# Kernel tuning notes

Measured on AMD Instinct MI355X. Metric: run time of the kernel, lower is better.

The kernel has to match this reference:

```python
import jax, jax.numpy as jnp
import numpy as np

B, C, H, W = 32, 3, 512, 512
OUT = (64, 64)  # (out_grid[0]=Nx, out_grid[1]=Ny)
SMALL = 1e-4


def setup_inputs() -> dict:
    key = jax.random.key(0)
    k1, k2 = jax.random.split(key, 2)
    X = jax.random.normal(k1, (B, C, H, W), dtype=jnp.float32)
    fan_in = C * H * W
    # localization net: flatten + dense(5); scaled so p ~ N(0,1) and exp(p) is stable
    W_loc = jax.random.normal(k2, (fan_in, 5), dtype=jnp.float32) / np.float32(np.sqrt(fan_in))
    b_loc = jnp.zeros((5,), dtype=jnp.float32)
    return {"X": X, "W_loc": W_loc, "b_loc": b_loc}


def reference(X, W_loc, b_loc):
    Bn = X.shape[0]
    # locnet: p = flatten(X) @ W_loc + b_loc  -> [B, 5]
    p = X.reshape(Bn, -1) @ W_loc + b_loc

    N = min(OUT)
    gx = OUT[0] * (p[:, 0] + 1.0) / 2.0          # [B]
    gy = OUT[1] * (p[:, 1] + 1.0) / 2.0          # [B]
    sigma2 = jnp.exp(p[:, 2])                    # [B]
    delta = jnp.exp(p[:, 3]) * (max(W, H) - 1) / (N - 1.0)  # [B]
    gamma = jnp.exp(p[:, 4])                     # [B]

    i1 = jnp.arange(OUT[0], dtype=jnp.float32)   # [Nx]
    i2 = jnp.arange(OUT[1], dtype=jnp.float32)   # [Ny]
    a = jnp.arange(W, dtype=jnp.float32)         # [W]
    b = jnp.arange(H, dtype=jnp.float32)         # [H]

    mx = gx[:, None] + delta[:, None] * (i1 - N / 2.0 - 0.5)  # [B, Nx]
    my = gy[:, None] + delta[:, None] * (i2 - N / 2.0 - 0.5)  # [B, Ny]

    Fx = jnp.exp(-((a - mx[:, :, None]) ** 2) / (2.0 * sigma2[:, None, None]))  # [B,Nx,W]
    Fx = Fx / (Fx.sum(axis=-1, keepdims=True) + SMALL)
    Fy = jnp.exp(-((b - my[:, :, None]) ** 2) / (2.0 * sigma2[:, None, None]))  # [B,Ny,H]
    Fy = Fy / (Fy.sum(axis=-1, keepdims=True) + SMALL)

    # glimpse read: gamma * Fy @ X @ Fx^T, done as batched contractions
    Fyx = jnp.einsum('bnh,bchw->bcnw', Fy, X)        # [B,C,Ny,W]
    out = jnp.einsum('bcnw,bmw->bcnm', Fyx, Fx)      # [B,C,Ny,Nx]
    return gamma[:, None, None, None] * out
```

## Files before the change

kernel.cpp:

```cpp
#include <hip/hip_runtime.h>
#include <math.h>

#define B_ 32
#define C_ 3
#define H_ 512
#define W_ 512
#define NOUT 64
#define FAN (C_*H_*W_)

#define CHUNKS 192
#define CELEMS (FAN / CHUNKS)
#define BGROUPS 4

#define PPART_STRIDE 160
#define GAMMA_OFF (CHUNKS * PPART_STRIDE)
#define PFLOATS 32768
#define FXH_U 0
#define FXL_U 1048576
#define FYH_U 2097152
#define FYL_U 3145728

typedef __bf16 bf16x8 __attribute__((ext_vector_type(8)));
typedef float f32x4 __attribute__((ext_vector_type(4)));

__device__ __forceinline__ unsigned short f2bf(float f) {
    unsigned int u = __float_as_uint(f);
    u = (u + 0x7FFFu + ((u >> 16) & 1u)) >> 16;
    return (unsigned short)u;
}
__device__ __forceinline__ float bf2f(unsigned short h) {
    return __uint_as_float(((unsigned int)h) << 16);
}
__device__ __forceinline__ unsigned int cvt_pk_bf16(float lo, float hi) {
    unsigned int r;
    asm("v_cvt_pk_bf16_f32 %0, %1, %2" : "=v"(r) : "v"(lo), "v"(hi));
    return r;
}

union BF8U { uint4 u; bf16x8 v; };

__global__ __launch_bounds__(256) void k_locnet(const float* __restrict__ X,
                                                const float* __restrict__ Wl,
                                                float* __restrict__ ws) {
    const int chunk = blockIdx.x;
    const int b0 = blockIdx.y * 8;
    const int t = threadIdx.x;

    float acc[8][5] = {};
    const size_t base = (size_t)chunk * CELEMS;

    for (int k = t; k < CELEMS / 4; k += 256) {
        const size_t i0 = base + (size_t)k * 4;
        const float4* W4 = (const float4*)(Wl + i0 * 5);
        float4 w0 = W4[0], w1 = W4[1], w2 = W4[2], w3 = W4[3], w4 = W4[4];
        float wv[20] = {w0.x, w0.y, w0.z, w0.w,
                        w1.x, w1.y, w1.z, w1.w,
                        w2.x, w2.y, w2.z, w2.w,
                        w3.x, w3.y, w3.z, w3.w,
                        w4.x, w4.y, w4.z, w4.w};
        #pragma unroll
        for (int bb = 0; bb < 8; bb++) {
            float4 x = *(const float4*)(X + (size_t)(b0 + bb) * FAN + i0);
            float xv[4] = {x.x, x.y, x.z, x.w};
            #pragma unroll
            for (int e = 0; e < 4; e++)
                #pragma unroll
                for (int j = 0; j < 5; j++)
                    acc[bb][j] += xv[e] * wv[e * 5 + j];
        }
    }

    #pragma unroll
    for (int off = 32; off > 0; off >>= 1)
        #pragma unroll
        for (int bb = 0; bb < 8; bb++)
            #pragma unroll
            for (int j = 0; j < 5; j++)
                acc[bb][j] += __shfl_down(acc[bb][j], off);

    __shared__ float sred[4][40];
    const int wave = t >> 6, lane = t & 63;
    if (lane == 0) {
        #pragma unroll
        for (int bb = 0; bb < 8; bb++)
            #pragma unroll
            for (int j = 0; j < 5; j++)
                sred[wave][bb * 5 + j] = acc[bb][j];
    }
    __syncthreads();
    if (t < 40) {
        float s = sred[0][t] + sred[1][t] + sred[2][t] + sred[3][t];
        ws[(size_t)chunk * PPART_STRIDE + b0 * 5 + t] = s;
    }
}

__global__ __launch_bounds__(256) void k_filters(const float* __restrict__ bl,
                                                 float* __restrict__ ws,
                                                 float* __restrict__ out) {
    const int n = blockIdx.x;
    const int b = blockIdx.y;
    const int which = blockIdx.z;
    const int t = threadIdx.x;

    {
        const int bid = blockIdx.x + NOUT * (blockIdx.y + B_ * blockIdx.z);
        if (t < 24) {
            ((float4*)out)[(size_t)bid * 24 + t] = make_float4(0.f, 0.f, 0.f, 0.f);
        }
    }

    float pj[5] = {0.f, 0.f, 0.f, 0.f, 0.f};
    if (t < CHUNKS) {
        const float* pr = ws + (size_t)t * PPART_STRIDE + b * 5;
        #pragma unroll
        for (int j = 0; j < 5; j++) pj[j] = pr[j];
    }
    #pragma unroll
    for (int off = 32; off > 0; off >>= 1)
        #pragma unroll
        for (int j = 0; j < 5; j++) pj[j] += __shfl_down(pj[j], off);

    __shared__ float spart[4][5];
    __shared__ float pfin[5];
    const int wave = t >> 6, lane = t & 63;
    if (lane == 0) {
        #pragma unroll
        for (int j = 0; j < 5; j++) spart[wave][j] = pj[j];
    }
    __syncthreads();
    if (t < 5) pfin[t] = spart[0][t] + spart[1][t] + spart[2][t] + spart[3][t] + bl[t];
    __syncthreads();

    const float p0 = pfin[0], p1 = pfin[1], p2 = pfin[2], p3 = pfin[3];
    if (which == 0 && n == 0 && t == 0) ws[GAMMA_OFF + b] = expf(pfin[4]);

    const float g = (which == 0) ? 32.f * (p0 + 1.f) : 32.f * (p1 + 1.f);
    const float sigma2 = expf(p2);
    const float inv2s = 0.5f / sigma2;
    const float delta = expf(p3) * (511.0f / 63.0f);
    const float mean = g + delta * ((float)n - 32.5f);

    float d0 = (float)(2 * t) - mean;
    float f0 = expf(-d0 * d0 * inv2s);
    float d1 = (float)(2 * t + 1) - mean;
    float f1 = expf(-d1 * d1 * inv2s);

    float s = f0 + f1;
    #pragma unroll
    for (int off = 32; off > 0; off >>= 1) s += __shfl_down(s, off);
    __shared__ float sred[4];
    __shared__ float stot;
    if (lane == 0) sred[wave] = s;
    __syncthreads();
    if (t == 0) stot = sred[0] + sred[1] + sred[2] + sred[3] + 1e-4f;
    __syncthreads();
    const float scale = 1.0f / stot;

    unsigned short* wsu = (unsigned short*)(ws + PFLOATS);
    unsigned int* dstH = (unsigned int*)(wsu + (which ? FYH_U : FXH_U) + ((size_t)b * NOUT + n) * 512);
    unsigned int* dstL = (unsigned int*)(wsu + (which ? FYL_U : FXL_U) + ((size_t)b * NOUT + n) * 512);

    float v0 = f0 * scale;
    float v1 = f1 * scale;
    unsigned short h0 = f2bf(v0);
    unsigned short h1 = f2bf(v1);
    unsigned short l0 = f2bf(v0 - bf2f(h0));
    unsigned short l1 = f2bf(v1 - bf2f(h1));
    dstH[t] = (unsigned int)h0 | ((unsigned int)h1 << 16);
    dstL[t] = (unsigned int)l0 | ((unsigned int)l1 << 16);
}

#define KC 64
#define PITCH 72
#define TSZ (64 * PITCH)

__global__ __launch_bounds__(256) void k_glimpse(const float* __restrict__ X,
                                                 const float* __restrict__ ws,
                                                 float* __restrict__ out) {
    const int hc = blockIdx.x;
    const int bc = blockIdx.y;
    const int b = bc / 3;
    const int t = threadIdx.x;
    const int lane = t & 63;
    const int wv = t >> 6;
    const int l15 = lane & 15;
    const int quad = lane >> 4;
    const int hbase = hc * 64;

    __shared__ __align__(16) unsigned short lds[4 * TSZ];
    unsigned short* Xh = lds;
    unsigned short* Xl = lds + TSZ;
    unsigned short* Fh = lds + 2 * TSZ;
    unsigned short* Fl = lds + 3 * TSZ;

    const float* Xp = X + (size_t)bc * (H_ * W_) + (size_t)hbase * W_;
    const unsigned short* wsu = (const unsigned short*)(ws + PFLOATS);
    const unsigned short* FxHp = wsu + FXH_U + (size_t)b * NOUT * 512;
    const unsigned short* FxLp = wsu + FXL_U + (size_t)b * NOUT * 512;
    const unsigned short* FyHp = wsu + FYH_U + (size_t)b * NOUT * 512;
    const unsigned short* FyLp = wsu + FYL_U + (size_t)b * NOUT * 512;

    const float* xlane = Xp + (size_t)(16 * wv + l15) * W_ + quad * 8;

    const int srow0 = t >> 3;
    const int sc8 = (t & 7) * 8;

    {
        uint4 h0 = *(const uint4*)(FxHp + (size_t)srow0 * 512 + sc8);
        uint4 l0 = *(const uint4*)(FxLp + (size_t)srow0 * 512 + sc8);
        uint4 h1 = *(const uint4*)(FxHp + (size_t)(srow0 + 32) * 512 + sc8);
        uint4 l1 = *(const uint4*)(FxLp + (size_t)(srow0 + 32) * 512 + sc8);
        *(uint4*)&Fh[srow0 * PITCH + sc8] = h0;
        *(uint4*)&Fl[srow0 * PITCH + sc8] = l0;
        *(uint4*)&Fh[(srow0 + 32) * PITCH + sc8] = h1;
        *(uint4*)&Fl[(srow0 + 32) * PITCH + sc8] = l1;
    }
    __syncthreads();

    f32x4 acc[4] = {};

    #pragma unroll
    for (int wt = 0; wt < 8; wt++) {
        unsigned short* curH = (wt & 1) ? Xh : Fh;
        unsigned short* curL = (wt & 1) ? Xl : Fl;
        unsigned short* nxtH = (wt & 1) ? Fh : Xh;
        unsigned short* nxtL = (wt & 1) ? Fl : Xl;

        uint4 nh0, nl0, nh1, nl1;
        if (wt < 7) {
            const int wb = (wt + 1) * KC;
            nh0 = *(const uint4*)(FxHp + (size_t)srow0 * 512 + wb + sc8);
            nl0 = *(const uint4*)(FxLp + (size_t)srow0 * 512 + wb + sc8);
            nh1 = *(const uint4*)(FxHp + (size_t)(srow0 + 32) * 512 + wb + sc8);
            nl1 = *(const uint4*)(FxLp + (size_t)(srow0 + 32) * 512 + wb + sc8);
        }

        #pragma unroll
        for (int ks = 0; ks < 2; ks++) {
            const float* xp = xlane + wt * KC + ks * 32;
            float4 x0 = *(const float4*)(xp);
            float4 x1 = *(const float4*)(xp + 4);
            BF8U ah, al;
            ah.u.x = cvt_pk_bf16(x0.x, x0.y);
            ah.u.y = cvt_pk_bf16(x0.z, x0.w);
            ah.u.z = cvt_pk_bf16(x1.x, x1.y);
            ah.u.w = cvt_pk_bf16(x1.z, x1.w);
            al.u.x = cvt_pk_bf16(x0.x - __uint_as_float(ah.u.x << 16),
                                 x0.y - __uint_as_float(ah.u.x & 0xffff0000u));
            al.u.y = cvt_pk_bf16(x0.z - __uint_as_float(ah.u.y << 16),
                                 x0.w - __uint_as_float(ah.u.y & 0xffff0000u));
            al.u.z = cvt_pk_bf16(x1.x - __uint_as_float(ah.u.z << 16),
                                 x1.y - __uint_as_float(ah.u.z & 0xffff0000u));
            al.u.w = cvt_pk_bf16(x1.z - __uint_as_float(ah.u.w << 16),
                                 x1.w - __uint_as_float(ah.u.w & 0xffff0000u));

            const int ko = ks * 32 + quad * 8;
            #pragma unroll
            for (int mt = 0; mt < 4; mt++) {
                bf16x8 bh = *(const bf16x8*)&curH[(16 * mt + l15) * PITCH + ko];
                bf16x8 bl2 = *(const bf16x8*)&curL[(16 * mt + l15) * PITCH + ko];
                acc[mt] = __builtin_amdgcn_mfma_f32_16x16x32_bf16(ah.v, bh, acc[mt], 0, 0, 0);
                acc[mt] = __builtin_amdgcn_mfma_f32_16x16x32_bf16(al.v, bh, acc[mt], 0, 0, 0);
                acc[mt] = __builtin_amdgcn_mfma_f32_16x16x32_bf16(ah.v, bl2, acc[mt], 0, 0, 0);
            }
        }

        if (wt < 7) {
            *(uint4*)&nxtH[srow0 * PITCH + sc8] = nh0;
            *(uint4*)&nxtL[srow0 * PITCH + sc8] = nl0;
            *(uint4*)&nxtH[(srow0 + 32) * PITCH + sc8] = nh1;
            *(uint4*)&nxtL[(srow0 + 32) * PITCH + sc8] = nl1;
        }
        __syncthreads();
    }

    #pragma unroll
    for (int mt = 0; mt < 4; mt++) {
        float g0 = acc[mt][0], g1 = acc[mt][1], g2 = acc[mt][2], g3 = acc[mt][3];
        unsigned int h01 = cvt_pk_bf16(g0, g1);
        unsigned int h23 = cvt_pk_bf16(g2, g3);
        float r0 = __uint_as_float(h01 << 16);
        float r1 = __uint_as_float(h01 & 0xffff0000u);
        float r2 = __uint_as_float(h23 << 16);
        float r3 = __uint_as_float(h23 & 0xffff0000u);
        unsigned int l01 = cvt_pk_bf16(g0 - r0, g1 - r1);
        unsigned int l23 = cvt_pk_bf16(g2 - r2, g3 - r3);
        int m = 16 * mt + l15;
        int h = 16 * wv + quad * 4;
        int o = m * PITCH + h;
        *(uint2*)&Xh[o] = make_uint2(h01, h23);
        *(uint2*)&Xl[o] = make_uint2(l01, l23);
    }

    {
        uint4 h0 = *(const uint4*)(FyHp + (size_t)srow0 * 512 + hbase + sc8);
        uint4 l0 = *(const uint4*)(FyLp + (size_t)srow0 * 512 + hbase + sc8);
        uint4 h1 = *(const uint4*)(FyHp + (size_t)(srow0 + 32) * 512 + hbase + sc8);
        uint4 l1 = *(const uint4*)(FyLp + (size_t)(srow0 + 32) * 512 + hbase + sc8);
        *(uint4*)&Fh[srow0 * PITCH + sc8] = h0;
        *(uint4*)&Fl[srow0 * PITCH + sc8] = l0;
        *(uint4*)&Fh[(srow0 + 32) * PITCH + sc8] = h1;
        *(uint4*)&Fl[(srow0 + 32) * PITCH + sc8] = l1;
    }
    __syncthreads();

    f32x4 p[4] = {};
    #pragma unroll
    for (int ks = 0; ks < 2; ks++) {
        const int ko = ks * 32 + quad * 8;
        bf16x8 yh = *(const bf16x8*)&Fh[(16 * wv + l15) * PITCH + ko];
        bf16x8 yl = *(const bf16x8*)&Fl[(16 * wv + l15) * PITCH + ko];
        #pragma unroll
        for (int mt = 0; mt < 4; mt++) {
            bf16x8 gh = *(const bf16x8*)&Xh[(16 * mt + l15) * PITCH + ko];
            bf16x8 gl = *(const bf16x8*)&Xl[(16 * mt + l15) * PITCH + ko];
            p[mt] = __builtin_amdgcn_mfma_f32_16x16x32_bf16(yh, gh, p[mt], 0, 0, 0);
            p[mt] = __builtin_amdgcn_mfma_f32_16x16x32_bf16(yl, gh, p[mt], 0, 0, 0);
            p[mt] = __builtin_amdgcn_mfma_f32_16x16x32_bf16(yh, gl, p[mt], 0, 0, 0);
        }
    }

    const float gamma = ws[GAMMA_OFF + b];
    float* outp = out + (size_t)bc * (NOUT * NOUT);
    #pragma unroll
    for (int mt = 0; mt < 4; mt++)
        #pragma unroll
        for (int r = 0; r < 4; r++) {
            int n = 16 * wv + quad * 4 + r;
            int m = 16 * mt + l15;
            atomicAdd(&outp[n * NOUT + m], gamma * p[mt][r]);
        }
}

extern "C" void kernel_launch(void* const* d_in, const int* in_sizes, int n_in,
                              void* d_out, int out_size, void* d_ws, size_t ws_size,
                              hipStream_t stream) {
    const float* X  = (const float*)d_in[0];
    const float* Wl = (const float*)d_in[1];
    const float* bl = (const float*)d_in[2];
    float* out = (float*)d_out;
    float* ws  = (float*)d_ws;

    k_locnet<<<dim3(CHUNKS, BGROUPS), 256, 0, stream>>>(X, Wl, ws);
    k_filters<<<dim3(NOUT, B_, 2), 256, 0, stream>>>(bl, ws, out);
    k_glimpse<<<dim3(8, B_ * C_), 256, 0, stream>>>(X, ws, out);
}
```

Measured before the change: 203.2 us.

## Split glimpse H-tiles to 32 rows and double locnet chunks for more blocks

The glimpse kernel now processes 32 H rows per block instead of 64, doubling the grid to 16x96 blocks. Each wave now handles one 16-row group and half of the output columns. The locnet reduction is split into 384 chunks, with the filter kernel summing two partials per thread. The aim is better CU occupancy on a grid that was small relative to the GPU. The cost is that Fx tiles are reloaded by twice as many blocks and twice as many output atomics are issued.

```diff
diff --git a/kernel.cpp b/kernel.cpp
--- a/kernel.cpp
+++ b/kernel.cpp
@@ -8,13 +8,13 @@
 #define NOUT 64
 #define FAN (C_*H_*W_)
 
-#define CHUNKS 192
+#define CHUNKS 384
 #define CELEMS (FAN / CHUNKS)
 #define BGROUPS 4
 
 #define PPART_STRIDE 160
 #define GAMMA_OFF (CHUNKS * PPART_STRIDE)
-#define PFLOATS 32768
+#define PFLOATS 65536
 #define FXH_U 0
 #define FXL_U 1048576
 #define FYH_U 2097152
@@ -109,11 +109,16 @@
         }
     }
 
-    float pj[5] = {0.f, 0.f, 0.f, 0.f, 0.f};
-    if (t < CHUNKS) {
+    float pj[5];
+    {
         const float* pr = ws + (size_t)t * PPART_STRIDE + b * 5;
         #pragma unroll
         for (int j = 0; j < 5; j++) pj[j] = pr[j];
+        if (t < CHUNKS - 256) {
+            const float* pr2 = ws + (size_t)(t + 256) * PPART_STRIDE + b * 5;
+            #pragma unroll
+            for (int j = 0; j < 5; j++) pj[j] += pr2[j];
+        }
     }
     #pragma unroll
     for (int off = 32; off > 0; off >>= 1)
@@ -171,6 +176,7 @@
 }
 
 #define KC 64
+#define HROWS 32
 #define PITCH 72
 #define TSZ (64 * PITCH)
 
@@ -185,7 +191,9 @@
     const int wv = t >> 6;
     const int l15 = lane & 15;
     const int quad = lane >> 4;
-    const int hbase = hc * 64;
+    const int rg = wv & 1;
+    const int mh = wv >> 1;
+    const int hbase = hc * HROWS;
 
     __shared__ __align__(16) unsigned short lds[4 * TSZ];
     unsigned short* Xh = lds;
@@ -200,7 +208,7 @@
     const unsigned short* FyHp = wsu + FYH_U + (size_t)b * NOUT * 512;
     const unsigned short* FyLp = wsu + FYL_U + (size_t)b * NOUT * 512;
 
-    const float* xlane = Xp + (size_t)(16 * wv + l15) * W_ + quad * 8;
+    const float* xlane = Xp + (size_t)(16 * rg + l15) * W_ + quad * 8;
 
     const int srow0 = t >> 3;
     const int sc8 = (t & 7) * 8;
@@ -217,7 +225,7 @@
     }
     __syncthreads();
 
-    f32x4 acc[4] = {};
+    f32x4 acc[2] = {};
 
     #pragma unroll
     for (int wt = 0; wt < 8; wt++) {
@@ -256,12 +264,13 @@
 
             const int ko = ks * 32 + quad * 8;
             #pragma unroll
-            for (int mt = 0; mt < 4; mt++) {
+            for (int j = 0; j < 2; j++) {
+                const int mt = 2 * mh + j;
                 bf16x8 bh = *(const bf16x8*)&curH[(16 * mt + l15) * PITCH + ko];
                 bf16x8 bl2 = *(const bf16x8*)&curL[(16 * mt + l15) * PITCH + ko];
-                acc[mt] = __builtin_amdgcn_mfma_f32_16x16x32_bf16(ah.v, bh, acc[mt], 0, 0, 0);
-                acc[mt] = __builtin_amdgcn_mfma_f32_16x16x32_bf16(al.v, bh, acc[mt], 0, 0, 0);
-                acc[mt] = __builtin_amdgcn_mfma_f32_16x16x32_bf16(ah.v, bl2, acc[mt], 0, 0, 0);
+                acc[j] = __builtin_amdgcn_mfma_f32_16x16x32_bf16(ah.v, bh, acc[j], 0, 0, 0);
+                acc[j] = __builtin_amdgcn_mfma_f32_16x16x32_bf16(al.v, bh, acc[j], 0, 0, 0);
+                acc[j] = __builtin_amdgcn_mfma_f32_16x16x32_bf16(ah.v, bl2, acc[j], 0, 0, 0);
             }
         }
 
@@ -275,8 +284,8 @@
     }
 
     #pragma unroll
-    for (int mt = 0; mt < 4; mt++) {
-        float g0 = acc[mt][0], g1 = acc[mt][1], g2 = acc[mt][2], g3 = acc[mt][3];
+    for (int j = 0; j < 2; j++) {
+        float g0 = acc[j][0], g1 = acc[j][1], g2 = acc[j][2], g3 = acc[j][3];
         unsigned int h01 = cvt_pk_bf16(g0, g1);
         unsigned int h23 = cvt_pk_bf16(g2, g3);
         float r0 = __uint_as_float(h01 << 16);
@@ -285,29 +294,26 @@
         float r3 = __uint_as_float(h23 & 0xffff0000u);
         unsigned int l01 = cvt_pk_bf16(g0 - r0, g1 - r1);
         unsigned int l23 = cvt_pk_bf16(g2 - r2, g3 - r3);
-        int m = 16 * mt + l15;
-        int h = 16 * wv + quad * 4;
+        int m = 16 * (2 * mh + j) + l15;
+        int h = 16 * rg + quad * 4;
         int o = m * PITCH + h;
         *(uint2*)&Xh[o] = make_uint2(h01, h23);
         *(uint2*)&Xl[o] = make_uint2(l01, l23);
     }
 
     {
-        uint4 h0 = *(const uint4*)(FyHp + (size_t)srow0 * 512 + hbase + sc8);
-        uint4 l0 = *(const uint4*)(FyLp + (size_t)srow0 * 512 + hbase + sc8);
-        uint4 h1 = *(const uint4*)(FyHp + (size_t)(srow0 + 32) * 512 + hbase + sc8);
-        uint4 l1 = *(const uint4*)(FyLp + (size_t)(srow0 + 32) * 512 + hbase + sc8);
-        *(uint4*)&Fh[srow0 * PITCH + sc8] = h0;
-        *(uint4*)&Fl[srow0 * PITCH + sc8] = l0;
-        *(uint4*)&Fh[(srow0 + 32) * PITCH + sc8] = h1;
-        *(uint4*)&Fl[(srow0 + 32) * PITCH + sc8] = l1;
+        const int frow = t >> 2;
+        const int fc8 = (t & 3) * 8;
+        uint4 h0 = *(const uint4*)(FyHp + (size_t)frow * 512 + hbase + fc8);
+        uint4 l0 = *(const uint4*)(FyLp + (size_t)frow * 512 + hbase + fc8);
+        *(uint4*)&Fh[frow * PITCH + fc8] = h0;
+        *(uint4*)&Fl[frow * PITCH + fc8] = l0;
     }
     __syncthreads();
 
     f32x4 p[4] = {};
-    #pragma unroll
-    for (int ks = 0; ks < 2; ks++) {
-        const int ko = ks * 32 + quad * 8;
+    {
+        const int ko = quad * 8;
         bf16x8 yh = *(const bf16x8*)&Fh[(16 * wv + l15) * PITCH + ko];
         bf16x8 yl = *(const bf16x8*)&Fl[(16 * wv + l15) * PITCH + ko];
         #pragma unroll
@@ -343,5 +349,5 @@
 
     k_locnet<<<dim3(CHUNKS, BGROUPS), 256, 0, stream>>>(X, Wl, ws);
     k_filters<<<dim3(NOUT, B_, 2), 256, 0, stream>>>(bl, ws, out);
-    k_glimpse<<<dim3(8, B_ * C_), 256, 0, stream>>>(X, ws, out);
-}
+    k_glimpse<<<dim3(16, B_ * C_), 256, 0, stream>>>(X, ws, out);
+}
```

After: 229.1 us. +12.7%, slower.

## Fuse locnet, filter and glimpse kernels into one persistent kernel with grid barriers

Applied to the files above, without the earlier changes.

Merges the three launches into a single 768-block kernel that runs the locnet reduction, the final parameter reduction, the filter construction and the glimpse matmuls as phases separated by software grid-wide barriers on an atomic counter in the workspace. The filter phase becomes a grid-stride loop over rows, and the per-batch parameter finalisation is done once by 32 blocks instead of redundantly in every filter block. This removes launch gaps and tail effects between kernels. In exchange it relies on all 768 blocks being co-resident (launch bounds request 4 blocks per CU), adds a memset for the barrier counters, and puts three grid barriers on the critical path.

```diff
diff --git a/kernel.cpp b/kernel.cpp
--- a/kernel.cpp
+++ b/kernel.cpp
@@ -10,10 +10,11 @@
 
 #define CHUNKS 192
 #define CELEMS (FAN / CHUNKS)
-#define BGROUPS 4
+#define GRID 768
 
 #define PPART_STRIDE 160
-#define GAMMA_OFF (CHUNKS * PPART_STRIDE)
+#define PF_OFF (CHUNKS * PPART_STRIDE)
+#define BAR_OFF 31000
 #define PFLOATS 32768
 #define FXH_U 0
 #define FXL_U 1048576
@@ -39,297 +40,323 @@
 
 union BF8U { uint4 u; bf16x8 v; };
 
-__global__ __launch_bounds__(256) void k_locnet(const float* __restrict__ X,
-                                                const float* __restrict__ Wl,
-                                                float* __restrict__ ws) {
-    const int chunk = blockIdx.x;
-    const int b0 = blockIdx.y * 8;
-    const int t = threadIdx.x;
-
-    float acc[8][5] = {};
-    const size_t base = (size_t)chunk * CELEMS;
-
-    for (int k = t; k < CELEMS / 4; k += 256) {
-        const size_t i0 = base + (size_t)k * 4;
-        const float4* W4 = (const float4*)(Wl + i0 * 5);
-        float4 w0 = W4[0], w1 = W4[1], w2 = W4[2], w3 = W4[3], w4 = W4[4];
-        float wv[20] = {w0.x, w0.y, w0.z, w0.w,
-                        w1.x, w1.y, w1.z, w1.w,
-                        w2.x, w2.y, w2.z, w2.w,
-                        w3.x, w3.y, w3.z, w3.w,
-                        w4.x, w4.y, w4.z, w4.w};
-        #pragma unroll
-        for (int bb = 0; bb < 8; bb++) {
-            float4 x = *(const float4*)(X + (size_t)(b0 + bb) * FAN + i0);
-            float xv[4] = {x.x, x.y, x.z, x.w};
-            #pragma unroll
-            for (int e = 0; e < 4; e++)
-                #pragma unroll
-                for (int j = 0; j < 5; j++)
-                    acc[bb][j] += xv[e] * wv[e * 5 + j];
-        }
-    }
-
-    #pragma unroll
-    for (int off = 32; off > 0; off >>= 1)
-        #pragma unroll
-        for (int bb = 0; bb < 8; bb++)
-            #pragma unroll
-            for (int j = 0; j < 5; j++)
-                acc[bb][j] += __shfl_down(acc[bb][j], off);
-
-    __shared__ float sred[4][40];
-    const int wave = t >> 6, lane = t & 63;
-    if (lane == 0) {
-        #pragma unroll
-        for (int bb = 0; bb < 8; bb++)
-            #pragma unroll
-            for (int j = 0; j < 5; j++)
-                sred[wave][bb * 5 + j] = acc[bb][j];
-    }
+__device__ __forceinline__ void grid_barrier(unsigned* bar, int t) {
     __syncthreads();
-    if (t < 40) {
-        float s = sred[0][t] + sred[1][t] + sred[2][t] + sred[3][t];
-        ws[(size_t)chunk * PPART_STRIDE + b0 * 5 + t] = s;
-    }
-}
-
-__global__ __launch_bounds__(256) void k_filters(const float* __restrict__ bl,
-                                                 float* __restrict__ ws,
-                                                 float* __restrict__ out) {
-    const int n = blockIdx.x;
-    const int b = blockIdx.y;
-    const int which = blockIdx.z;
-    const int t = threadIdx.x;
-
-    {
-        const int bid = blockIdx.x + NOUT * (blockIdx.y + B_ * blockIdx.z);
-        if (t < 24) {
-            ((float4*)out)[(size_t)bid * 24 + t] = make_float4(0.f, 0.f, 0.f, 0.f);
-        }
-    }
-
-    float pj[5] = {0.f, 0.f, 0.f, 0.f, 0.f};
-    if (t < CHUNKS) {
-        const float* pr = ws + (size_t)t * PPART_STRIDE + b * 5;
-        #pragma unroll
-        for (int j = 0; j < 5; j++) pj[j] = pr[j];
-    }
-    #pragma unroll
-    for (int off = 32; off > 0; off >>= 1)
-        #pragma unroll
-        for (int j = 0; j < 5; j++) pj[j] += __shfl_down(pj[j], off);
-
-    __shared__ float spart[4][5];
-    __shared__ float pfin[5];
-    const int wave = t >> 6, lane = t & 63;
-    if (lane == 0) {
-        #pragma unroll
-        for (int j = 0; j < 5; j++) spart[wave][j] = pj[j];
+    if (t == 0) {
+        unsigned g = __hip_atomic_load(&bar[1], __ATOMIC_RELAXED, __HIP_MEMORY_SCOPE_AGENT);
+        __threadfence();
+        unsigned arrived = __hip_atomic_fetch_add(&bar[0], 1u, __ATOMIC_ACQ_REL,
+                                                  __HIP_MEMORY_SCOPE_AGENT) + 1u;
+        if (arrived == (unsigned)GRID) {
+            __hip_atomic_store(&bar[0], 0u, __ATOMIC_RELAXED, __HIP_MEMORY_SCOPE_AGENT);
+            __hip_atomic_fetch_add(&bar[1], 1u, __ATOMIC_RELEASE, __HIP_MEMORY_SCOPE_AGENT);
+        } else {
+            long cap = 0;
+            while (__hip_atomic_load(&bar[1], __ATOMIC_ACQUIRE,
+                                     __HIP_MEMORY_SCOPE_AGENT) == g) {
+                if (++cap > (1L << 31)) break;
+            }
+        }
+        __threadfence();
     }
     __syncthreads();
-    if (t < 5) pfin[t] = spart[0][t] + spart[1][t] + spart[2][t] + spart[3][t] + bl[t];
-    __syncthreads();
-
-    const float p0 = pfin[0], p1 = pfin[1], p2 = pfin[2], p3 = pfin[3];
-    if (which == 0 && n == 0 && t == 0) ws[GAMMA_OFF + b] = expf(pfin[4]);
-
-    const float g = (which == 0) ? 32.f * (p0 + 1.f) : 32.f * (p1 + 1.f);
-    const float sigma2 = expf(p2);
-    const float inv2s = 0.5f / sigma2;
-    const float delta = expf(p3) * (511.0f / 63.0f);
-    const float mean = g + delta * ((float)n - 32.5f);
-
-    float d0 = (float)(2 * t) - mean;
-    float f0 = expf(-d0 * d0 * inv2s);
-    float d1 = (float)(2 * t + 1) - mean;
-    float f1 = expf(-d1 * d1 * inv2s);
-
-    float s = f0 + f1;
-    #pragma unroll
-    for (int off = 32; off > 0; off >>= 1) s += __shfl_down(s, off);
-    __shared__ float sred[4];
-    __shared__ float stot;
-    if (lane == 0) sred[wave] = s;
-    __syncthreads();
-    if (t == 0) stot = sred[0] + sred[1] + sred[2] + sred[3] + 1e-4f;
-    __syncthreads();
-    const float scale = 1.0f / stot;
-
-    unsigned short* wsu = (unsigned short*)(ws + PFLOATS);
-    unsigned int* dstH = (unsigned int*)(wsu + (which ? FYH_U : FXH_U) + ((size_t)b * NOUT + n) * 512);
-    unsigned int* dstL = (unsigned int*)(wsu + (which ? FYL_U : FXL_U) + ((size_t)b * NOUT + n) * 512);
-
-    float v0 = f0 * scale;
-    float v1 = f1 * scale;
-    unsigned short h0 = f2bf(v0);
-    unsigned short h1 = f2bf(v1);
-    unsigned short l0 = f2bf(v0 - bf2f(h0));
-    unsigned short l1 = f2bf(v1 - bf2f(h1));
-    dstH[t] = (unsigned int)h0 | ((unsigned int)h1 << 16);
-    dstL[t] = (unsigned int)l0 | ((unsigned int)l1 << 16);
 }
 
 #define KC 64
 #define PITCH 72
 #define TSZ (64 * PITCH)
 
-__global__ __launch_bounds__(256) void k_glimpse(const float* __restrict__ X,
-                                                 const float* __restrict__ ws,
-                                                 float* __restrict__ out) {
-    const int hc = blockIdx.x;
-    const int bc = blockIdx.y;
-    const int b = bc / 3;
+__global__ __launch_bounds__(256, 4) void k_fused(const float* __restrict__ X,
+                                                  const float* __restrict__ Wl,
+                                                  const float* __restrict__ bl,
+                                                  float* __restrict__ ws,
+                                                  float* __restrict__ out) {
+    const int bid = blockIdx.x;
     const int t = threadIdx.x;
     const int lane = t & 63;
-    const int wv = t >> 6;
-    const int l15 = lane & 15;
-    const int quad = lane >> 4;
-    const int hbase = hc * 64;
+    const int wave = t >> 6;
+    unsigned* bar = (unsigned*)(ws + BAR_OFF);
 
     __shared__ __align__(16) unsigned short lds[4 * TSZ];
-    unsigned short* Xh = lds;
-    unsigned short* Xl = lds + TSZ;
-    unsigned short* Fh = lds + 2 * TSZ;
-    unsigned short* Fl = lds + 3 * TSZ;
-
-    const float* Xp = X + (size_t)bc * (H_ * W_) + (size_t)hbase * W_;
-    const unsigned short* wsu = (const unsigned short*)(ws + PFLOATS);
-    const unsigned short* FxHp = wsu + FXH_U + (size_t)b * NOUT * 512;
-    const unsigned short* FxLp = wsu + FXL_U + (size_t)b * NOUT * 512;
-    const unsigned short* FyHp = wsu + FYH_U + (size_t)b * NOUT * 512;
-    const unsigned short* FyLp = wsu + FYL_U + (size_t)b * NOUT * 512;
-
-    const float* xlane = Xp + (size_t)(16 * wv + l15) * W_ + quad * 8;
-
-    const int srow0 = t >> 3;
-    const int sc8 = (t & 7) * 8;
+    __shared__ float sred[4][40];
+    __shared__ float sredB[4];
+    __shared__ float stot;
 
     {
-        uint4 h0 = *(const uint4*)(FxHp + (size_t)srow0 * 512 + sc8);
-        uint4 l0 = *(const uint4*)(FxLp + (size_t)srow0 * 512 + sc8);
-        uint4 h1 = *(const uint4*)(FxHp + (size_t)(srow0 + 32) * 512 + sc8);
-        uint4 l1 = *(const uint4*)(FxLp + (size_t)(srow0 + 32) * 512 + sc8);
-        *(uint4*)&Fh[srow0 * PITCH + sc8] = h0;
-        *(uint4*)&Fl[srow0 * PITCH + sc8] = l0;
-        *(uint4*)&Fh[(srow0 + 32) * PITCH + sc8] = h1;
-        *(uint4*)&Fl[(srow0 + 32) * PITCH + sc8] = l1;
-    }
-    __syncthreads();
-
-    f32x4 acc[4] = {};
-
-    #pragma unroll
-    for (int wt = 0; wt < 8; wt++) {
-        unsigned short* curH = (wt & 1) ? Xh : Fh;
-        unsigned short* curL = (wt & 1) ? Xl : Fl;
-        unsigned short* nxtH = (wt & 1) ? Fh : Xh;
-        unsigned short* nxtL = (wt & 1) ? Fl : Xl;
-
-        uint4 nh0, nl0, nh1, nl1;
-        if (wt < 7) {
-            const int wb = (wt + 1) * KC;
-            nh0 = *(const uint4*)(FxHp + (size_t)srow0 * 512 + wb + sc8);
-            nl0 = *(const uint4*)(FxLp + (size_t)srow0 * 512 + wb + sc8);
-            nh1 = *(const uint4*)(FxHp + (size_t)(srow0 + 32) * 512 + wb + sc8);
-            nl1 = *(const uint4*)(FxLp + (size_t)(srow0 + 32) * 512 + wb + sc8);
-        }
-
+        const int chunk = bid >> 2;
+        const int b0 = (bid & 3) * 8;
+        float acc[8][5] = {};
+        const size_t base = (size_t)chunk * CELEMS;
+
+        for (int k = t; k < CELEMS / 4; k += 256) {
+            const size_t i0 = base + (size_t)k * 4;
+            const float4* W4 = (const float4*)(Wl + i0 * 5);
+            float4 w0 = W4[0], w1 = W4[1], w2 = W4[2], w3 = W4[3], w4 = W4[4];
+            float wv[20] = {w0.x, w0.y, w0.z, w0.w,
+                            w1.x, w1.y, w1.z, w1.w,
+                            w2.x, w2.y, w2.z, w2.w,
+                            w3.x, w3.y, w3.z, w3.w,
+                            w4.x, w4.y, w4.z, w4.w};
+            #pragma unroll
+            for (int bb = 0; bb < 8; bb++) {
+                float4 x = *(const float4*)(X + (size_t)(b0 + bb) * FAN + i0);
+                float xv[4] = {x.x, x.y, x.z, x.w};
+                #pragma unroll
+                for (int e = 0; e < 4; e++)
+                    #pragma unroll
+                    for (int j = 0; j < 5; j++)
+                        acc[bb][j] += xv[e] * wv[e * 5 + j];
+            }
+        }
+
+        #pragma unroll
+        for (int off = 32; off > 0; off >>= 1)
+            #pragma unroll
+            for (int bb = 0; bb < 8; bb++)
+                #pragma unroll
+                for (int j = 0; j < 5; j++)
+                    acc[bb][j] += __shfl_down(acc[bb][j], off);
+
+        if (lane == 0) {
+            #pragma unroll
+            for (int bb = 0; bb < 8; bb++)
+                #pragma unroll
+                for (int j = 0; j < 5; j++)
+                    sred[wave][bb * 5 + j] = acc[bb][j];
+        }
+        __syncthreads();
+        if (t < 40) {
+            float s = sred[0][t] + sred[1][t] + sred[2][t] + sred[3][t];
+            ws[(size_t)chunk * PPART_STRIDE + b0 * 5 + t] = s;
+        }
+    }
+    grid_barrier(bar, t);
+
+    if (bid < B_) {
+        const int b = bid;
+        float pj[5] = {0.f, 0.f, 0.f, 0.f, 0.f};
+        if (t < CHUNKS) {
+            const float* pr = ws + (size_t)t * PPART_STRIDE + b * 5;
+            #pragma unroll
+            for (int j = 0; j < 5; j++) pj[j] = pr[j];
+        }
+        #pragma unroll
+        for (int off = 32; off > 0; off >>= 1)
+            #pragma unroll
+            for (int j = 0; j < 5; j++) pj[j] += __shfl_down(pj[j], off);
+        if (lane == 0) {
+            #pragma unroll
+            for (int j = 0; j < 5; j++) sred[wave][j] = pj[j];
+        }
+        __syncthreads();
+        if (t < 5) {
+            float v = sred[0][t] + sred[1][t] + sred[2][t] + sred[3][t] + bl[t];
+            ws[PF_OFF + b * 8 + t] = (t == 4) ? expf(v) : v;
+        }
+    }
+    grid_barrier(bar, t);
+
+    for (int u = bid; u < 2 * B_ * NOUT; u += GRID) {
+        const int which = u >> 11;
+        const int b = (u >> 6) & 31;
+        const int n = u & 63;
+
+        if (t < 24)
+            ((float4*)out)[(size_t)u * 24 + t] = make_float4(0.f, 0.f, 0.f, 0.f);
+
+        const float p0 = ws[PF_OFF + b * 8 + 0];
+        const float p1 = ws[PF_OFF + b * 8 + 1];
+        const float p2 = ws[PF_OFF + b * 8 + 2];
+        const float p3 = ws[PF_OFF + b * 8 + 3];
+
+        const float g = (which == 0) ? 32.f * (p0 + 1.f) : 32.f * (p1 + 1.f);
+        const float sigma2 = expf(p2);
+        const float inv2s = 0.5f / sigma2;
+        const float delta = expf(p3) * (511.0f / 63.0f);
+        const float mean = g + delta * ((float)n - 32.5f);
+
+        float d0 = (float)(2 * t) - mean;
+        float f0 = expf(-d0 * d0 * inv2s);
+        float d1 = (float)(2 * t + 1) - mean;
+        float f1 = expf(-d1 * d1 * inv2s);
+
+        float s = f0 + f1;
+        #pragma unroll
+        for (int off = 32; off > 0; off >>= 1) s += __shfl_down(s, off);
+        if (lane == 0) sredB[wave] = s;
+        __syncthreads();
+        if (t == 0) stot = sredB[0] + sredB[1] + sredB[2] + sredB[3] + 1e-4f;
+        __syncthreads();
+        const float scale = 1.0f / stot;
+
+        unsigned short* wsu = (unsigned short*)(ws + PFLOATS);
+        unsigned int* dstH = (unsigned int*)(wsu + (which ? FYH_U : FXH_U) + ((size_t)b * NOUT + n) * 512);
+        unsigned int* dstL = (unsigned int*)(wsu + (which ? FYL_U : FXL_U) + ((size_t)b * NOUT + n) * 512);
+
+        float v0 = f0 * scale;
+        float v1 = f1 * scale;
+        unsigned short h0 = f2bf(v0);
+        unsigned short h1 = f2bf(v1);
+        unsigned short l0 = f2bf(v0 - bf2f(h0));
+        unsigned short l1 = f2bf(v1 - bf2f(h1));
+        dstH[t] = (unsigned int)h0 | ((unsigned int)h1 << 16);
+        dstL[t] = (unsigned int)l0 | ((unsigned int)l1 << 16);
+        __syncthreads();
+    }
+    grid_barrier(bar, t);
+
+    {
+        const int hc = bid & 7;
+        const int bc = bid >> 3;
+        const int b = bc / 3;
+        const int wv = wave;
+        const int l15 = lane & 15;
+        const int quad = lane >> 4;
+        const int hbase = hc * 64;
+
+        unsigned short* Xh = lds;
+        unsigned short* Xl = lds + TSZ;
+        unsigned short* Fh = lds + 2 * TSZ;
+        unsigned short* Fl = lds + 3 * TSZ;
+
+        const float* Xp = X + (size_t)bc * (H_ * W_) + (size_t)hbase * W_;
+        const unsigned short* wsu = (const unsigned short*)(ws + PFLOATS);
+        const unsigned short* FxHp = wsu + FXH_U + (size_t)b * NOUT * 512;
+        const unsigned short* FxLp = wsu + FXL_U + (size_t)b * NOUT * 512;
+        const unsigned short* FyHp = wsu + FYH_U + (size_t)b * NOUT * 512;
+        const unsigned short* FyLp = wsu + FYL_U + (size_t)b * NOUT * 512;
+
+        const float* xlane = Xp + (size_t)(16 * wv + l15) * W_ + quad * 8;
+
+        const int srow0 = t >> 3;
+        const int sc8 = (t & 7) * 8;
+
+        {
+            uint4 h0 = *(const uint4*)(FxHp + (size_t)srow0 * 512 + sc8);
+            uint4 l0 = *(const uint4*)(FxLp + (size_t)srow0 * 512 + sc8);
+            uint4 h1 = *(const uint4*)(FxHp + (size_t)(srow0 + 32) * 512 + sc8);
+            uint4 l1 = *(const uint4*)(FxLp + (size_t)(srow0 + 32) * 512 + sc8);
+            *(uint4*)&Fh[srow0 * PITCH + sc8] = h0;
+            *(uint4*)&Fl[srow0 * PITCH + sc8] = l0;
+            *(uint4*)&Fh[(srow0 + 32) * PITCH + sc8] = h1;
+            *(uint4*)&Fl[(srow0 + 32) * PITCH + sc8] = l1;
+        }
+        __syncthreads();
+
+        f32x4 acc[4] = {};
+
+        #pragma unroll
+        for (int wt = 0; wt < 8; wt++) {
+            unsigned short* curH = (wt & 1) ? Xh : Fh;
+            unsigned short* curL = (wt & 1) ? Xl : Fl;
+            unsigned short* nxtH = (wt & 1) ? Fh : Xh;
+            unsigned short* nxtL = (wt & 1) ? Fl : Xl;
+
+            uint4 nh0, nl0, nh1, nl1;
+            if (wt < 7) {
+                const int wb = (wt + 1) * KC;
+                nh0 = *(const uint4*)(FxHp + (size_t)srow0 * 512 + wb + sc8);
+                nl0 = *(const uint4*)(FxLp + (size_t)srow0 * 512 + wb + sc8);
+                nh1 = *(const uint4*)(FxHp + (size_t)(srow0 + 32) * 512 + wb + sc8);
+                nl1 = *(const uint4*)(FxLp + (size_t)(srow0 + 32) * 512 + wb + sc8);
+            }
+
+            #pragma unroll
+            for (int ks = 0; ks < 2; ks++) {
+                const float* xp = xlane + wt * KC + ks * 32;
+                float4 x0 = *(const float4*)(xp);
+                float4 x1 = *(const float4*)(xp + 4);
+                BF8U ah, al;
+                ah.u.x = cvt_pk_bf16(x0.x, x0.y);
+                ah.u.y = cvt_pk_bf16(x0.z, x0.w);
+                ah.u.z = cvt_pk_bf16(x1.x, x1.y);
+                ah.u.w = cvt_pk_bf16(x1.z, x1.w);
+                al.u.x = cvt_pk_bf16(x0.x - __uint_as_float(ah.u.x << 16),
+                                     x0.y - __uint_as_float(ah.u.x & 0xffff0000u));
+                al.u.y = cvt_pk_bf16(x0.z - __uint_as_float(ah.u.y << 16),
+                                     x0.w - __uint_as_float(ah.u.y & 0xffff0000u));
+                al.u.z = cvt_pk_bf16(x1.x - __uint_as_float(ah.u.z << 16),
+                                     x1.y - __uint_as_float(ah.u.z & 0xffff0000u));
+                al.u.w = cvt_pk_bf16(x1.z - __uint_as_float(ah.u.w << 16),
+                                     x1.w - __uint_as_float(ah.u.w & 0xffff0000u));
+
+                const int ko = ks * 32 + quad * 8;
+                #pragma unroll
+                for (int mt = 0; mt < 4; mt++) {
+                    bf16x8 bh = *(const bf16x8*)&curH[(16 * mt + l15) * PITCH + ko];
+                    bf16x8 bl2 = *(const bf16x8*)&curL[(16 * mt + l15) * PITCH + ko];
+                    acc[mt] = __builtin_amdgcn_mfma_f32_16x16x32_bf16(ah.v, bh, acc[mt], 0, 0, 0);
+                    acc[mt] = __builtin_amdgcn_mfma_f32_16x16x32_bf16(al.v, bh, acc[mt], 0, 0, 0);
+                    acc[mt] = __builtin_amdgcn_mfma_f32_16x16x32_bf16(ah.v, bl2, acc[mt], 0, 0, 0);
+                }
+            }
+
+            if (wt < 7) {
+                *(uint4*)&nxtH[srow0 * PITCH + sc8] = nh0;
+                *(uint4*)&nxtL[srow0 * PITCH + sc8] = nl0;
+                *(uint4*)&nxtH[(srow0 + 32) * PITCH + sc8] = nh1;
+                *(uint4*)&nxtL[(srow0 + 32) * PITCH + sc8] = nl1;
+            }
+            __syncthreads();
+        }
+
+        #pragma unroll
+        for (int mt = 0; mt < 4; mt++) {
+            float g0 = acc[mt][0], g1 = acc[mt][1], g2 = acc[mt][2], g3 = acc[mt][3];
+            unsigned int h01 = cvt_pk_bf16(g0, g1);
+            unsigned int h23 = cvt_pk_bf16(g2, g3);
+            float r0 = __uint_as_float(h01 << 16);
+            float r1 = __uint_as_float(h01 & 0xffff0000u);
+            float r2 = __uint_as_float(h23 << 16);
+            float r3 = __uint_as_float(h23 & 0xffff0000u);
+            unsigned int l01 = cvt_pk_bf16(g0 - r0, g1 - r1);
+            unsigned int l23 = cvt_pk_bf16(g2 - r2, g3 - r3);
+            int m = 16 * mt + l15;
+            int h = 16 * wv + quad * 4;
+            int o = m * PITCH + h;
+            *(uint2*)&Xh[o] = make_uint2(h01, h23);
+            *(uint2*)&Xl[o] = make_uint2(l01, l23);
+        }
+
+        {
+            uint4 h0 = *(const uint4*)(FyHp + (size_t)srow0 * 512 + hbase + sc8);
+            uint4 l0 = *(const uint4*)(FyLp + (size_t)srow0 * 512 + hbase + sc8);
+            uint4 h1 = *(const uint4*)(FyHp + (size_t)(srow0 + 32) * 512 + hbase + sc8);
+            uint4 l1 = *(const uint4*)(FyLp + (size_t)(srow0 + 32) * 512 + hbase + sc8);
+            *(uint4*)&Fh[srow0 * PITCH + sc8] = h0;
+            *(uint4*)&Fl[srow0 * PITCH + sc8] = l0;
+            *(uint4*)&Fh[(srow0 + 32) * PITCH + sc8] = h1;
+            *(uint4*)&Fl[(srow0 + 32) * PITCH + sc8] = l1;
+        }
+        __syncthreads();
+
+        f32x4 p[4] = {};
         #pragma unroll
         for (int ks = 0; ks < 2; ks++) {
-            const float* xp = xlane + wt * KC + ks * 32;
-            float4 x0 = *(const float4*)(xp);
-            float4 x1 = *(const float4*)(xp + 4);
-            BF8U ah, al;
-            ah.u.x = cvt_pk_bf16(x0.x, x0.y);
-            ah.u.y = cvt_pk_bf16(x0.z, x0.w);
-            ah.u.z = cvt_pk_bf16(x1.x, x1.y);
-            ah.u.w = cvt_pk_bf16(x1.z, x1.w);
-            al.u.x = cvt_pk_bf16(x0.x - __uint_as_float(ah.u.x << 16),
-                                 x0.y - __uint_as_float(ah.u.x & 0xffff0000u));
-            al.u.y = cvt_pk_bf16(x0.z - __uint_as_float(ah.u.y << 16),
-                                 x0.w - __uint_as_float(ah.u.y & 0xffff0000u));
-            al.u.z = cvt_pk_bf16(x1.x - __uint_as_float(ah.u.z << 16),
-                                 x1.y - __uint_as_float(ah.u.z & 0xffff0000u));
-            al.u.w = cvt_pk_bf16(x1.z - __uint_as_float(ah.u.w << 16),
-                                 x1.w - __uint_as_float(ah.u.w & 0xffff0000u));
-
             const int ko = ks * 32 + quad * 8;
+            bf16x8 yh = *(const bf16x8*)&Fh[(16 * wv + l15) * PITCH + ko];
+            bf16x8 yl = *(const bf16x8*)&Fl[(16 * wv + l15) * PITCH + ko];
             #pragma unroll
             for (int mt = 0; mt < 4; mt++) {
-                bf16x8 bh = *(const bf16x8*)&curH[(16 * mt + l15) * PITCH + ko];
-                bf16x8 bl2 = *(const bf16x8*)&curL[(16 * mt + l15) * PITCH + ko];
-                acc[mt] = __builtin_amdgcn_mfma_f32_16x16x32_bf16(ah.v, bh, acc[mt], 0, 0, 0);
-                acc[mt] = __builtin_amdgcn_mfma_f32_16x16x32_bf16(al.v, bh, acc[mt], 0, 0, 0);
-                acc[mt] = __builtin_amdgcn_mfma_f32_16x16x32_bf16(ah.v, bl2, acc[mt], 0, 0, 0);
-            }
-        }
-
-        if (wt < 7) {
-            *(uint4*)&nxtH[srow0 * PITCH + sc8] = nh0;
-            *(uint4*)&nxtL[srow0 * PITCH + sc8] = nl0;
-            *(uint4*)&nxtH[(srow0 + 32) * PITCH + sc8] = nh1;
-            *(uint4*)&nxtL[(srow0 + 32) * PITCH + sc8] = nl1;
-        }
-        __syncthreads();
-    }
-
-    #pragma unroll
-    for (int mt = 0; mt < 4; mt++) {
-        float g0 = acc[mt][0], g1 = acc[mt][1], g2 = acc[mt][2], g3 = acc[mt][3];
-        unsigned int h01 = cvt_pk_bf16(g0, g1);
-        unsigned int h23 = cvt_pk_bf16(g2, g3);
-        float r0 = __uint_as_float(h01 << 16);
-        float r1 = __uint_as_float(h01 & 0xffff0000u);
-        float r2 = __uint_as_float(h23 << 16);
-        float r3 = __uint_as_float(h23 & 0xffff0000u);
-        unsigned int l01 = cvt_pk_bf16(g0 - r0, g1 - r1);
-        unsigned int l23 = cvt_pk_bf16(g2 - r2, g3 - r3);
-        int m = 16 * mt + l15;
-        int h = 16 * wv + quad * 4;
-        int o = m * PITCH + h;
-        *(uint2*)&Xh[o] = make_uint2(h01, h23);
-        *(uint2*)&Xl[o] = make_uint2(l01, l23);
-    }
-
-    {
-        uint4 h0 = *(const uint4*)(FyHp + (size_t)srow0 * 512 + hbase + sc8);
-        uint4 l0 = *(const uint4*)(FyLp + (size_t)srow0 * 512 + hbase + sc8);
-        uint4 h1 = *(const uint4*)(FyHp + (size_t)(srow0 + 32) * 512 + hbase + sc8);
-        uint4 l1 = *(const uint4*)(FyLp + (size_t)(srow0 + 32) * 512 + hbase + sc8);
-        *(uint4*)&Fh[srow0 * PITCH + sc8] = h0;
-        *(uint4*)&Fl[srow0 * PITCH + sc8] = l0;
-        *(uint4*)&Fh[(srow0 + 32) * PITCH + sc8] = h1;
-        *(uint4*)&Fl[(srow0 + 32) * PITCH + sc8] = l1;
-    }
-    __syncthreads();
-
-    f32x4 p[4] = {};
-    #pragma unroll
-    for (int ks = 0; ks < 2; ks++) {
-        const int ko = ks * 32 + quad * 8;
-        bf16x8 yh = *(const bf16x8*)&Fh[(16 * wv + l15) * PITCH + ko];
-        bf16x8 yl = *(const bf16x8*)&Fl[(16 * wv + l15) * PITCH + ko];
-        #pragma unroll
-        for (int mt = 0; mt < 4; mt++) {
-            bf16x8 gh = *(const bf16x8*)&Xh[(16 * mt + l15) * PITCH + ko];
-            bf16x8 gl = *(const bf16x8*)&Xl[(16 * mt + l15) * PITCH + ko];
-            p[mt] = __builtin_amdgcn_mfma_f32_16x16x32_bf16(yh, gh, p[mt], 0, 0, 0);
-            p[mt] = __builtin_amdgcn_mfma_f32_16x16x32_bf16(yl, gh, p[mt], 0, 0, 0);
-            p[mt] = __builtin_amdgcn_mfma_f32_16x16x32_bf16(yh, gl, p[mt], 0, 0, 0);
-        }
-    }
-
-    const float gamma = ws[GAMMA_OFF + b];
-    float* outp = out + (size_t)bc * (NOUT * NOUT);
-    #pragma unroll
-    for (int mt = 0; mt < 4; mt++)
-        #pragma unroll
-        for (int r = 0; r < 4; r++) {
-            int n = 16 * wv + quad * 4 + r;
-            int m = 16 * mt + l15;
-            atomicAdd(&outp[n * NOUT + m], gamma * p[mt][r]);
-        }
+                bf16x8 gh = *(const bf16x8*)&Xh[(16 * mt + l15) * PITCH + ko];
+                bf16x8 gl = *(const bf16x8*)&Xl[(16 * mt + l15) * PITCH + ko];
+                p[mt] = __builtin_amdgcn_mfma_f32_16x16x32_bf16(yh, gh, p[mt], 0, 0, 0);
+                p[mt] = __builtin_amdgcn_mfma_f32_16x16x32_bf16(yl, gh, p[mt], 0, 0, 0);
+                p[mt] = __builtin_amdgcn_mfma_f32_16x16x32_bf16(yh, gl, p[mt], 0, 0, 0);
+            }
+        }
+
+        const float gamma = ws[PF_OFF + b * 8 + 4];
+        float* outp = out + (size_t)bc * (NOUT * NOUT);
+        #pragma unroll
+        for (int mt = 0; mt < 4; mt++)
+            #pragma unroll
+            for (int r = 0; r < 4; r++) {
+                int n = 16 * wv + quad * 4 + r;
+                int m = 16 * mt + l15;
+                atomicAdd(&outp[n * NOUT + m], gamma * p[mt][r]);
+            }
+    }
 }
 
 extern "C" void kernel_launch(void* const* d_in, const int* in_sizes, int n_in,
@@ -341,7 +368,7 @@
     float* out = (float*)d_out;
     float* ws  = (float*)d_ws;
 
-    k_locnet<<<dim3(CHUNKS, BGROUPS), 256, 0, stream>>>(X, Wl, ws);
-    k_filters<<<dim3(NOUT, B_, 2), 256, 0, stream>>>(bl, ws, out);
-    k_glimpse<<<dim3(8, B_ * C_), 256, 0, stream>>>(X, ws, out);
-}
+    hipMemsetAsync((char*)ws + BAR_OFF * sizeof(float), 0, 2 * sizeof(unsigned), stream);
+
+    k_fused<<<dim3(GRID), dim3(256), 0, stream>>>(X, Wl, bl, ws, out);
+}
```

New measurement: 513.9 us. +153.0%, slower.
